# Optimization experiments

Hardware: AMD Instinct MI355X
Metric: run time of the kernel (lower is better)

The kernel has to match this reference:

```python
import jax, jax.numpy as jnp
import numpy as np

B, CIN, COUT, HIN = 2, 64, 64, 96
ALPHA = 0.2       # LeakyReLU slope in GAT
K_RANK = 6        # dist.argsort(1).argsort(1) <= 6  -> 7 nearest neighbors incl. self
DN = ('NCHW', 'OIHW', 'NCHW')


def setup_inputs():
    key = jax.random.key(0)
    ks = jax.random.split(key, 10)
    sc = lambda k, shape, s: jax.random.normal(k, shape, jnp.float32) * s
    return {
        'x': jax.random.normal(ks[0], (B, CIN, HIN, HIN), jnp.float32),
        'conv_w': sc(ks[1], (COUT, CIN, 3, 3), 0.05),
        'conv_b': jnp.zeros((COUT,), jnp.float32),
        'W1': sc(ks[2], (COUT, COUT), 0.1),
        'a1': sc(ks[3], (2 * COUT,), 0.1),
        'W2': sc(ks[4], (COUT, COUT), 0.1),
        'a2': sc(ks[5], (2 * COUT,), 0.1),
        'Wout': sc(ks[6], (2 * COUT, COUT), 0.1),
        'aout': sc(ks[7], (2 * COUT,), 0.1),
        'tconv_w': sc(ks[8], (COUT, COUT, 3, 3), 0.05),  # torch ConvTranspose2d layout [in,out,kh,kw]
        'tconv_b': jnp.zeros((COUT,), jnp.float32),
    }


def _gat_layer(h, adj, W, a, concat):
    # h: [B,N,F_in], W: [F_in,F_out], a: [2*F_out]
    Wh = h @ W                                   # [B,N,F']
    Fo = W.shape[1]
    e = (Wh @ a[:Fo])[:, :, None] + (Wh @ a[Fo:])[:, None, :]   # [B,N,N]
    e = jax.nn.leaky_relu(e, ALPHA)
    e = jnp.where(adj > 0, e, -9e15)
    attn = jax.nn.softmax(e, axis=-1)
    out = jnp.einsum('bij,bjf->bif', attn, Wh)
    return jax.nn.elu(out) if concat else out


def reference(x, conv_w, conv_b, W1, a1, W2, a2, Wout, aout, tconv_w, tconv_b):
    # --- Pre_ProcessLayer_Graph: stride-2 conv, flatten, 7-NN dense adjacency ---
    y = jax.lax.conv_general_dilated(x, conv_w, (2, 2), ((1, 1), (1, 1)),
                                     dimension_numbers=DN) + conv_b[None, :, None, None]
    Bb, C, H, W_ = y.shape
    N = H * W_
    feat = y.reshape(Bb, C, N).transpose(0, 2, 1)          # [B,N,C]
    sq = jnp.sum(feat * feat, axis=-1)                     # [B,N]
    d2 = sq[:, :, None] + sq[:, None, :] - 2.0 * jnp.einsum('bic,bjc->bij', feat, feat)
    dist = jnp.sqrt(jnp.maximum(d2, 0.0))                  # euclidean cdist
    ranks = jnp.argsort(jnp.argsort(dist, axis=-1), axis=-1)
    adj = (ranks <= K_RANK).astype(feat.dtype)             # [B,N,N] binary, incl. self (rank 0)
    # --- GAT (pyGAT style): 2 concat heads + output attention layer, eval mode ---
    h1 = _gat_layer(feat, adj, W1, a1, True)
    h2 = _gat_layer(feat, adj, W2, a2, True)
    hcat = jnp.concatenate([h1, h2], axis=-1)              # [B,N,2C]
    g = jax.nn.elu(_gat_layer(hcat, adj, Wout, aout, False))  # [B,N,C]
    # --- reshape back + transpose conv (k=3, s=2, p=1, output_padding=1) ---
    g = g.transpose(0, 2, 1).reshape(Bb, C, H, W_)
    wt = jnp.flip(tconv_w, (2, 3)).transpose(1, 0, 2, 3)   # -> [out,in,kh,kw]
    out = jax.lax.conv_general_dilated(g, wt, (1, 1), ((1, 2), (1, 2)),
                                       lhs_dilation=(2, 2),
                                       dimension_numbers=DN) + tconv_b[None, :, None, None]
    return out
```

## Files before the change

### kernel.cpp

```cpp
#include <hip/hip_runtime.h>
#include <hip/hip_bf16.h>
#include <stdint.h>

using bf16 = __hip_bfloat16;
using u64 = unsigned long long;

constexpr int B_ = 2;
constexpr int N_ = 2304;

constexpr int OFF_WC2   = 0;
constexpr int OFF_WT2   = 36864;
constexpr int OFF_W1F   = 73728;
constexpr int OFF_W2F   = 77824;
constexpr int OFF_WOUTF = 81920;
constexpr int OFF_A1F   = 90112;
constexpr int OFF_A2F   = 90240;
constexpr int OFF_AOUTF = 90368;
constexpr int OFF_CBF   = 90496;
constexpr int OFF_TBF   = 90560;
constexpr int OFF_FLAG  = 90624;
constexpr int OFF_SQ    = 90688;
constexpr int OFF_S11   = 95296;
constexpr int OFF_S12   = 99904;
constexpr int OFF_S21   = 104512;
constexpr int OFF_S22   = 109120;
constexpr int OFF_S1O   = 113728;
constexpr int OFF_S2O   = 118336;
constexpr int OFF_KNN   = 122944;
constexpr int OFF_BUF0  = 159808;
constexpr int OFF_BUF1  = 454720;
constexpr int OFF_BUF2  = 749632;
constexpr int OFF_BUF3  = 1044544;
constexpr int OFF_PK    = 1339456;

__device__ __forceinline__ float bf2f_raw(unsigned short u) {
    return __uint_as_float(((unsigned int)u) << 16);
}

__device__ __forceinline__ unsigned int mono32(float f) {
    unsigned int u = __float_as_uint(f);
    return (u & 0x80000000u) ? ~u : (u | 0x80000000u);
}

__device__ __forceinline__ bool detect_f32(const void* conv_w) {
    const unsigned short* cw = (const unsigned short*)conv_w;
    float m = 0.f;
    #pragma unroll
    for (int u = 0; u < 64; ++u) {
        float v = fabsf(bf2f_raw(cw[u]));
        if (v < 3.0e38f) m = fmaxf(m, v);
    }
    return m > 1.0e4f;
}

__global__ __launch_bounds__(256) void kc_prep(
    const void* conv_w, const void* conv_b, const void* W1, const void* a1,
    const void* W2, const void* a2, const void* Wout, const void* aout,
    const void* tconv_w, const void* tconv_b, float* __restrict__ ws)
{
    bool f32 = detect_f32(conv_w);
    int idx = blockIdx.x * 256 + threadIdx.x;
    if (idx == 0) ws[OFF_FLAG] = f32 ? 1.f : 0.f;
    if (idx < 32256) ws[OFF_SQ + idx] = 0.f;

    {
        int tap = idx >> 12, ic = (idx >> 6) & 63, oc = idx & 63;
        if (f32) {
            ws[OFF_WC2 + idx] = ((const float*)conv_w)[(oc * 64 + ic) * 9 + tap];
            ws[OFF_WT2 + idx] = ((const float*)tconv_w)[(ic * 64 + oc) * 9 + tap];
        } else {
            ws[OFF_WC2 + idx] = bf2f_raw(((const unsigned short*)conv_w)[(oc * 64 + ic) * 9 + tap]);
            ws[OFF_WT2 + idx] = bf2f_raw(((const unsigned short*)tconv_w)[(ic * 64 + oc) * 9 + tap]);
        }
    }
    if (idx < 4096) {
        if (f32) {
            ws[OFF_W1F + idx] = ((const float*)W1)[idx];
            ws[OFF_W2F + idx] = ((const float*)W2)[idx];
        } else {
            ws[OFF_W1F + idx] = bf2f_raw(((const unsigned short*)W1)[idx]);
            ws[OFF_W2F + idx] = bf2f_raw(((const unsigned short*)W2)[idx]);
        }
    }
    if (idx < 8192)
        ws[OFF_WOUTF + idx] = f32 ? ((const float*)Wout)[idx]
                                  : bf2f_raw(((const unsigned short*)Wout)[idx]);
    if (idx < 128) {
        if (f32) {
            ws[OFF_A1F + idx]   = ((const float*)a1)[idx];
            ws[OFF_A2F + idx]   = ((const float*)a2)[idx];
            ws[OFF_AOUTF + idx] = ((const float*)aout)[idx];
        } else {
            ws[OFF_A1F + idx]   = bf2f_raw(((const unsigned short*)a1)[idx]);
            ws[OFF_A2F + idx]   = bf2f_raw(((const unsigned short*)a2)[idx]);
            ws[OFF_AOUTF + idx] = bf2f_raw(((const unsigned short*)aout)[idx]);
        }
    }
    if (idx < 64) {
        if (f32) {
            ws[OFF_CBF + idx] = ((const float*)conv_b)[idx];
            ws[OFF_TBF + idx] = ((const float*)tconv_b)[idx];
        } else {
            ws[OFF_CBF + idx] = bf2f_raw(((const unsigned short*)conv_b)[idx]);
            ws[OFF_TBF + idx] = bf2f_raw(((const unsigned short*)tconv_b)[idx]);
        }
    }
}

template <bool F32>
__device__ __forceinline__ void conv_body(const void* __restrict__ x,
                                          float* __restrict__ ws,
                                          int n, int ocb, int b)
{
    int oy = n / 48, ox = n - (n / 48) * 48;
    const float* wc2 = ws + OFF_WC2;
    size_t xb = (size_t)b * 64 * 9216;
    float acc[4] = {0, 0, 0, 0};

    for (int ky = 0; ky < 3; ++ky) {
        int iy = 2 * oy - 1 + ky;
        bool vy = (unsigned)iy < 96u;
        int iyc = vy ? iy : 0;
        for (int kx = 0; kx < 3; ++kx) {
            int ix = 2 * ox - 1 + kx;
            bool v = vy && ((unsigned)ix < 96u);
            int ixc = v ? ix : 0;
            size_t xoff = xb + iyc * 96 + ixc;
            const float* wb = wc2 + (ky * 3 + kx) * 4096 + ocb;
            #pragma unroll 8
            for (int ic = 0; ic < 64; ++ic) {
                float xv;
                if (F32) xv = ((const float*)x)[xoff + ic * 9216];
                else     xv = bf2f_raw(((const unsigned short*)x)[xoff + ic * 9216]);
                xv = v ? xv : 0.f;
                const float* wr = wb + ic * 64;
                #pragma unroll
                for (int o = 0; o < 4; ++o) acc[o] += xv * wr[o];
            }
        }
    }
    float* featT = ws + OFF_BUF0 + (size_t)b * 64 * N_;
    const float* cb = ws + OFF_CBF;
    float ssum = 0.f;
    #pragma unroll
    for (int o = 0; o < 4; ++o) {
        float f = acc[o] + cb[ocb + o];
        acc[o] = f;
        featT[(ocb + o) * N_ + n] = f;
        ssum += f * f;
    }
    *(float4*)(ws + OFF_BUF2 + ((size_t)(b * N_ + n) * 64 + ocb)) =
        make_float4(acc[0], acc[1], acc[2], acc[3]);
    atomicAdd(ws + OFF_SQ + b * N_ + n, ssum);
}

__global__ __launch_bounds__(128) void k1_conv(const void* __restrict__ x,
                                               float* __restrict__ ws)
{
    int n   = blockIdx.x * 128 + threadIdx.x;
    int ocb = blockIdx.y * 4;
    int b   = blockIdx.z;
    if (ws[OFF_FLAG] != 0.f) conv_body<true >(x, ws, n, ocb, b);
    else                     conv_body<false>(x, ws, n, ocb, b);
}

__global__ __launch_bounds__(256) void k2_knn(float* __restrict__ ws)
{
    __shared__ float Bs[32][256];
    float* ysp = &Bs[0][0];
    int tid = threadIdx.x;
    int i0  = blockIdx.x * 16;
    int jh  = blockIdx.y;
    int b   = i0 / N_;
    const float* fT  = ws + OFF_BUF0 + (size_t)b * 64 * N_;
    const float* fnc = ws + OFF_BUF2;
    const float* sq  = ws + OFF_SQ + b * N_;
    int w = tid >> 6, lane = tid & 63;
    int r0 = w * 4;
    int arow0 = __builtin_amdgcn_readfirstlane(i0 + r0);

    u64 K[7];
    #pragma unroll
    for (int t = 0; t < 7; ++t) K[t] = ~0ull;

    int rsel = tid >> 4;
    int g    = tid & 15;

    for (int jt = 0; jt < 3; ++jt) {
        int jb = jh * 768 + jt * 256;
        float acc[4][4];
        #pragma unroll
        for (int r = 0; r < 4; ++r)
            #pragma unroll
            for (int c = 0; c < 4; ++c) acc[r][c] = 0.f;

        for (int kh = 0; kh < 2; ++kh) {
            __syncthreads();
            #pragma unroll
            for (int it = 0; it < 8; ++it) {
                int idx = tid + it * 256;
                int k = idx >> 6, j4 = idx & 63;
                float4 v = *(const float4*)(fT + (size_t)(kh * 32 + k) * N_ + jb + j4 * 4);
                *(float4*)&Bs[k][j4 * 4] = v;
            }
            __syncthreads();

            #pragma unroll 2
            for (int k4 = 0; k4 < 8; ++k4) {
                float4 Bv[4];
                #pragma unroll
                for (int kk = 0; kk < 4; ++kk)
                    Bv[kk] = *(const float4*)&Bs[k4 * 4 + kk][4 * lane];
                #pragma unroll
                for (int r = 0; r < 4; ++r) {
                    float4 a = *(const float4*)(fnc + (size_t)(arow0 + r) * 64
                                                + kh * 32 + k4 * 4);
                    acc[r][0] += a.x * Bv[0].x + a.y * Bv[1].x + a.z * Bv[2].x + a.w * Bv[3].x;
                    acc[r][1] += a.x * Bv[0].y + a.y * Bv[1].y + a.z * Bv[2].y + a.w * Bv[3].y;
                    acc[r][2] += a.x * Bv[0].z + a.y * Bv[1].z + a.z * Bv[2].z + a.w * Bv[3].z;
                    acc[r][3] += a.x * Bv[0].w + a.y * Bv[1].w + a.z * Bv[2].w + a.w * Bv[3].w;
                }
            }
        }

        __syncthreads();
        float4 sqv = *(const float4*)(sq + jb + 4 * lane);
        #pragma unroll
        for (int r = 0; r < 4; ++r) {
            float4 yv;
            yv.x = sqv.x - 2.f * acc[r][0];
            yv.y = sqv.y - 2.f * acc[r][1];
            yv.z = sqv.z - 2.f * acc[r][2];
            yv.w = sqv.w - 2.f * acc[r][3];
            *(float4*)&ysp[(r0 + r) * 264 + 4 * lane] = yv;
        }
        __syncthreads();

        #pragma unroll 4
        for (int u = 0; u < 16; ++u) {
            int jl = g + 16 * u;
            float y = ysp[rsel * 264 + jl];
            u64 key = ((u64)mono32(y) << 32) | (unsigned int)(jb + jl);
            if (key < K[6]) {
                int pos = 0;
                #pragma unroll
                for (int s = 0; s < 7; ++s) pos += (K[s] < key) ? 1 : 0;
                #pragma unroll
                for (int p = 6; p > 0; --p)
                    K[p] = (p == pos) ? key : ((p > pos) ? K[p - 1] : K[p]);
                if (pos == 0) K[0] = key;
            }
        }
        __syncthreads();
    }

    u64 myk = 0;
    for (int pass = 0; pass < 7; ++pass) {
        u64 m = K[0];
        #pragma unroll
        for (int s = 1; s < 7; ++s) m = (K[s] < m) ? K[s] : m;
        #pragma unroll
        for (int off = 1; off < 16; off <<= 1) {
            u64 o = (u64)__shfl_xor((long long)m, off);
            m = (o < m) ? o : m;
        }
        #pragma unroll
        for (int s = 0; s < 7; ++s)
            if (K[s] == m) K[s] = ~0ull;
        if (g == pass) myk = m;
    }
    if (g < 7) {
        u64* pk = (u64*)(ws + OFF_PK);
        pk[((size_t)(i0 + rsel) * 3 + jh) * 8 + g] = myk;
    }
}

__global__ __launch_bounds__(256) void k_lin(float* __restrict__ ws)
{
    int g = blockIdx.y;
    if (g == 32) {
        int row = blockIdx.x * 256 + threadIdx.x;
        const u64* pk = (const u64*)(ws + OFF_PK) + (size_t)row * 24;
        int* kout = (int*)(ws + OFF_KNN) + (size_t)row * 8;
        u64 L0[7], L1[7], L2[7];
        #pragma unroll
        for (int q = 0; q < 7; ++q) { L0[q] = pk[q]; L1[q] = pk[8 + q]; L2[q] = pk[16 + q]; }
        #pragma unroll
        for (int q = 0; q < 7; ++q) {
            int rank = q;
            #pragma unroll
            for (int p = 0; p < 7; ++p)
                rank += ((L1[p] < L0[q]) ? 1 : 0) + ((L2[p] < L0[q]) ? 1 : 0);
            if (rank < 7) kout[rank] = (int)(L0[q] & 0xffffffffull);
        }
        #pragma unroll
        for (int q = 0; q < 7; ++q) {
            int rank = q;
            #pragma unroll
            for (int p = 0; p < 7; ++p)
                rank += ((L0[p] < L1[q]) ? 1 : 0) + ((L2[p] < L1[q]) ? 1 : 0);
            if (rank < 7) kout[rank] = (int)(L1[q] & 0xffffffffull);
        }
        #pragma unroll
        for (int q = 0; q < 7; ++q) {
            int rank = q;
            #pragma unroll
            for (int p = 0; p < 7; ++p)
                rank += ((L0[p] < L2[q]) ? 1 : 0) + ((L1[p] < L2[q]) ? 1 : 0);
            if (rank < 7) kout[rank] = (int)(L2[q] & 0xffffffffull);
        }
        return;
    }
    int layer = g >> 4;
    int ocb = (g & 15) * 4;
    const float* W  = ws + (layer ? OFF_W2F : OFF_W1F);
    const float* a  = ws + (layer ? OFF_A2F : OFF_A1F);
    float* out_nc   = ws + (layer ? OFF_BUF3 : OFF_BUF1);
    float* s1       = ws + (layer ? OFF_S21 : OFF_S11);
    float* s2       = ws + (layer ? OFF_S22 : OFF_S12);
    int i = blockIdx.x * 256 + threadIdx.x;
    int b = i / N_, n = i - b * N_;
    const float* in_b = ws + OFF_BUF0 + (size_t)b * 64 * N_;

    float acc[4] = {0, 0, 0, 0};
    #pragma unroll 8
    for (int kk = 0; kk < 64; ++kk) {
        float xv = in_b[kk * N_ + n];
        const float* wr = W + kk * 64 + ocb;
        #pragma unroll
        for (int o = 0; o < 4; ++o) acc[o] += xv * wr[o];
    }
    *(float4*)(out_nc + ((size_t)i * 64 + ocb)) =
        make_float4(acc[0], acc[1], acc[2], acc[3]);
    float p1 = 0.f, p2 = 0.f;
    #pragma unroll
    for (int o = 0; o < 4; ++o) {
        p1 += acc[o] * a[ocb + o];
        p2 += acc[o] * a[64 + ocb + o];
    }
    atomicAdd(s1 + i, p1);
    atomicAdd(s2 + i, p2);
}

__global__ __launch_bounds__(256) void k_lin2(float* __restrict__ ws)
{
    int ocb = blockIdx.y * 4;
    int i = blockIdx.x * 256 + threadIdx.x;
    int b = i / N_, n = i - b * N_;
    const float* h1 = ws + OFF_BUF2 + (size_t)b * 64 * N_;
    const float* h2 = ws + OFF_BUF0 + (size_t)b * 64 * N_;
    const float* W  = ws + OFF_WOUTF;
    const float* a  = ws + OFF_AOUTF;

    float acc[4] = {0, 0, 0, 0};
    #pragma unroll 8
    for (int kk = 0; kk < 64; ++kk) {
        float xv = h1[kk * N_ + n];
        const float* wr = W + kk * 64 + ocb;
        #pragma unroll
        for (int o = 0; o < 4; ++o) acc[o] += xv * wr[o];
    }
    #pragma unroll 8
    for (int kk = 0; kk < 64; ++kk) {
        float xv = h2[kk * N_ + n];
        const float* wr = W + (64 + kk) * 64 + ocb;
        #pragma unroll
        for (int o = 0; o < 4; ++o) acc[o] += xv * wr[o];
    }
    *(float4*)(ws + OFF_BUF1 + ((size_t)i * 64 + ocb)) =
        make_float4(acc[0], acc[1], acc[2], acc[3]);
    float p1 = 0.f, p2 = 0.f;
    #pragma unroll
    for (int o = 0; o < 4; ++o) {
        p1 += acc[o] * a[ocb + o];
        p2 += acc[o] * a[64 + ocb + o];
    }
    atomicAdd(ws + OFF_S1O + i, p1);
    atomicAdd(ws + OFF_S2O + i, p2);
}

__device__ __forceinline__ void attn_body(
    const float* __restrict__ Wh_nc, const float* __restrict__ s1,
    const float* __restrict__ s2, const int* __restrict__ knn,
    float* __restrict__ out, int i, int b, int n, int c4)
{
    const int* kp = knn + (size_t)i * 8;
    int j[7];
    #pragma unroll
    for (int t = 0; t < 7; ++t) {
        int jt = kp[t];
        j[t] = ((unsigned)jt < (unsigned)N_) ? jt : 0;
    }
    float si = s1[i];
    const float* s2b = s2 + b * N_;
    float e[7];
    #pragma unroll
    for (int t = 0; t < 7; ++t) {
        float v = si + s2b[j[t]];
        e[t] = v > 0.f ? v : 0.2f * v;
    }
    float m = e[0];
    #pragma unroll
    for (int t = 1; t < 7; ++t) m = fmaxf(m, e[t]);
    float ssum = 0.f;
    #pragma unroll
    for (int t = 0; t < 7; ++t) { e[t] = __expf(e[t] - m); ssum += e[t]; }
    float inv = 1.f / ssum;
    #pragma unroll
    for (int t = 0; t < 7; ++t) e[t] *= inv;

    const float4* W4 = (const float4*)Wh_nc;
    float4 acc = make_float4(0.f, 0.f, 0.f, 0.f);
    #pragma unroll
    for (int t = 0; t < 7; ++t) {
        float4 v = W4[(size_t)(b * N_ + j[t]) * 16 + c4];
        acc.x += e[t] * v.x; acc.y += e[t] * v.y;
        acc.z += e[t] * v.z; acc.w += e[t] * v.w;
    }
    acc.x = acc.x > 0.f ? acc.x : expm1f(acc.x);
    acc.y = acc.y > 0.f ? acc.y : expm1f(acc.y);
    acc.z = acc.z > 0.f ? acc.z : expm1f(acc.z);
    acc.w = acc.w > 0.f ? acc.w : expm1f(acc.w);
    float* ob = out + (size_t)b * 64 * N_;
    ob[(c4 * 4 + 0) * N_ + n] = acc.x;
    ob[(c4 * 4 + 1) * N_ + n] = acc.y;
    ob[(c4 * 4 + 2) * N_ + n] = acc.z;
    ob[(c4 * 4 + 3) * N_ + n] = acc.w;
}

__global__ __launch_bounds__(256) void k_attn12(float* __restrict__ ws)
{
    int layer = blockIdx.z;
    const float* Wh_nc = ws + (layer ? OFF_BUF3 : OFF_BUF1);
    const float* s1    = ws + (layer ? OFF_S21 : OFF_S11);
    const float* s2    = ws + (layer ? OFF_S22 : OFF_S12);
    float* out         = ws + (layer ? OFF_BUF0 : OFF_BUF2);
    int c4 = blockIdx.y;
    int i = blockIdx.x * 256 + threadIdx.x;
    int b = i / N_, n = i - b * N_;
    attn_body(Wh_nc, s1, s2, (const int*)(ws + OFF_KNN), out, i, b, n, c4);
}

__global__ __launch_bounds__(256) void k_attn_out(float* __restrict__ ws)
{
    int c4 = blockIdx.y;
    int i = blockIdx.x * 256 + threadIdx.x;
    int b = i / N_, n = i - b * N_;
    attn_body(ws + OFF_BUF1, ws + OFF_S1O, ws + OFF_S2O,
              (const int*)(ws + OFF_KNN), ws + OFF_BUF3, i, b, n, c4);
}

__global__ __launch_bounds__(128) void k7_tconv(float* __restrict__ ws,
                                                void* __restrict__ outp)
{
    bool f32 = ws[OFF_FLAG] != 0.f;
    int pixc = blockIdx.x * 128 + threadIdx.x;
    int g    = blockIdx.y;
    int pc   = g >> 3, ocb = (g & 7) * 8;
    int b    = blockIdx.z;
    int py = pc >> 1, px = pc & 1;
    int ay = pixc / 48, bx = pixc - (pixc / 48) * 48;
    int oy = 2 * ay + py, ox = 2 * bx + px;

    const float* gT  = ws + OFF_BUF3 + (size_t)b * 64 * N_;
    const float* wt2 = ws + OFF_WT2;
    float acc[8] = {0, 0, 0, 0, 0, 0, 0, 0};

    int nky = py ? 2 : 1;
    int nkx = px ? 2 : 1;
    for (int s = 0; s < nky; ++s) {
        int ky = py ? (s == 0 ? 0 : 2) : 1;
        int iy = py ? (s == 0 ? ay + 1 : ay) : ay;
        bool vy = iy < 48;
        for (int t = 0; t < nkx; ++t) {
            int kx = px ? (t == 0 ? 0 : 2) : 1;
            int ix = px ? (t == 0 ? bx + 1 : bx) : bx;
            bool v = vy && (ix < 48);
            const float* gp = gT + (v ? iy * 48 + ix : 0);
            const float* wb = wt2 + (ky * 3 + kx) * 4096 + ocb;
            #pragma unroll 8
            for (int ic = 0; ic < 64; ++ic) {
                float gv = gp[ic * N_];
                gv = v ? gv : 0.f;
                const float* wr = wb + ic * 64;
                #pragma unroll
                for (int o = 0; o < 8; ++o) acc[o] += gv * wr[o];
            }
        }
    }
    const float* tb = ws + OFF_TBF;
    size_t base = ((size_t)(b * 64 + ocb) * 96 + oy) * 96 + ox;
    if (f32) {
        float* op = (float*)outp;
        #pragma unroll
        for (int o = 0; o < 8; ++o) op[base + (size_t)o * 9216] = acc[o] + tb[ocb + o];
    } else {
        bf16* op = (bf16*)outp;
        #pragma unroll
        for (int o = 0; o < 8; ++o)
            op[base + (size_t)o * 9216] = __float2bfloat16(acc[o] + tb[ocb + o]);
    }
}

extern "C" void kernel_launch(void* const* d_in, const int* in_sizes, int n_in,
                              void* d_out, int out_size, void* d_ws, size_t ws_size,
                              hipStream_t stream)
{
    float* ws = (float*)d_ws;

    hipLaunchKernelGGL(kc_prep, dim3(144), dim3(256), 0, stream,
                       d_in[1], d_in[2], d_in[3], d_in[4], d_in[5], d_in[6],
                       d_in[7], d_in[8], d_in[9], d_in[10], ws);
    hipLaunchKernelGGL(k1_conv, dim3(18, 16, 2), dim3(128), 0, stream, d_in[0], ws);
    hipLaunchKernelGGL(k2_knn, dim3(288, 3), dim3(256), 0, stream, ws);
    hipLaunchKernelGGL(k_lin, dim3(18, 33), dim3(256), 0, stream, ws);
    hipLaunchKernelGGL(k_attn12, dim3(18, 16, 2), dim3(256), 0, stream, ws);
    hipLaunchKernelGGL(k_lin2, dim3(18, 16), dim3(256), 0, stream, ws);
    hipLaunchKernelGGL(k_attn_out, dim3(18, 16), dim3(256), 0, stream, ws);
    hipLaunchKernelGGL(k7_tconv, dim3(18, 32, 2), dim3(128), 0, stream, ws, d_out);
}
```

Before: 230.7 us.

## Fuse all stages into one persistent kernel with atomic grid barriers

```diff
diff --git a/kernel.cpp b/kernel.cpp
--- a/kernel.cpp
+++ b/kernel.cpp
@@ -19,6 +19,7 @@
 constexpr int OFF_CBF   = 90496;
 constexpr int OFF_TBF   = 90560;
 constexpr int OFF_FLAG  = 90624;
+constexpr int OFF_BAR   = 90632;
 constexpr int OFF_SQ    = 90688;
 constexpr int OFF_S11   = 95296;
 constexpr int OFF_S12   = 99904;
@@ -33,6 +34,8 @@
 constexpr int OFF_BUF3  = 1044544;
 constexpr int OFF_PK    = 1339456;
 
+constexpr unsigned NBLK = 864;
+
 __device__ __forceinline__ float bf2f_raw(unsigned short u) {
     return __uint_as_float(((unsigned int)u) << 16);
 }
@@ -53,67 +56,27 @@
     return m > 1.0e4f;
 }
 
-__global__ __launch_bounds__(256) void kc_prep(
-    const void* conv_w, const void* conv_b, const void* W1, const void* a1,
-    const void* W2, const void* a2, const void* Wout, const void* aout,
-    const void* tconv_w, const void* tconv_b, float* __restrict__ ws)
-{
-    bool f32 = detect_f32(conv_w);
-    int idx = blockIdx.x * 256 + threadIdx.x;
-    if (idx == 0) ws[OFF_FLAG] = f32 ? 1.f : 0.f;
-    if (idx < 32256) ws[OFF_SQ + idx] = 0.f;
-
-    {
-        int tap = idx >> 12, ic = (idx >> 6) & 63, oc = idx & 63;
-        if (f32) {
-            ws[OFF_WC2 + idx] = ((const float*)conv_w)[(oc * 64 + ic) * 9 + tap];
-            ws[OFF_WT2 + idx] = ((const float*)tconv_w)[(ic * 64 + oc) * 9 + tap];
-        } else {
-            ws[OFF_WC2 + idx] = bf2f_raw(((const unsigned short*)conv_w)[(oc * 64 + ic) * 9 + tap]);
-            ws[OFF_WT2 + idx] = bf2f_raw(((const unsigned short*)tconv_w)[(ic * 64 + oc) * 9 + tap]);
-        }
-    }
-    if (idx < 4096) {
-        if (f32) {
-            ws[OFF_W1F + idx] = ((const float*)W1)[idx];
-            ws[OFF_W2F + idx] = ((const float*)W2)[idx];
-        } else {
-            ws[OFF_W1F + idx] = bf2f_raw(((const unsigned short*)W1)[idx]);
-            ws[OFF_W2F + idx] = bf2f_raw(((const unsigned short*)W2)[idx]);
-        }
-    }
-    if (idx < 8192)
-        ws[OFF_WOUTF + idx] = f32 ? ((const float*)Wout)[idx]
-                                  : bf2f_raw(((const unsigned short*)Wout)[idx]);
-    if (idx < 128) {
-        if (f32) {
-            ws[OFF_A1F + idx]   = ((const float*)a1)[idx];
-            ws[OFF_A2F + idx]   = ((const float*)a2)[idx];
-            ws[OFF_AOUTF + idx] = ((const float*)aout)[idx];
-        } else {
-            ws[OFF_A1F + idx]   = bf2f_raw(((const unsigned short*)a1)[idx]);
-            ws[OFF_A2F + idx]   = bf2f_raw(((const unsigned short*)a2)[idx]);
-            ws[OFF_AOUTF + idx] = bf2f_raw(((const unsigned short*)aout)[idx]);
-        }
-    }
-    if (idx < 64) {
-        if (f32) {
-            ws[OFF_CBF + idx] = ((const float*)conv_b)[idx];
-            ws[OFF_TBF + idx] = ((const float*)tconv_b)[idx];
-        } else {
-            ws[OFF_CBF + idx] = bf2f_raw(((const unsigned short*)conv_b)[idx]);
-            ws[OFF_TBF + idx] = bf2f_raw(((const unsigned short*)tconv_b)[idx]);
-        }
-    }
+__device__ __forceinline__ void gridbar(float* __restrict__ ws, unsigned target) {
+    __syncthreads();
+    if (threadIdx.x == 0) {
+        __threadfence();
+        atomicAdd((unsigned*)(ws + OFF_BAR), 1u);
+        int guard = 0;
+        while (atomicAdd((unsigned*)(ws + OFF_BAR), 0u) < target) {
+            __builtin_amdgcn_s_sleep(32);
+            if (++guard > (1 << 20)) break;
+        }
+        __threadfence();
+    }
+    __syncthreads();
 }
 
 template <bool F32>
-__device__ __forceinline__ void conv_body(const void* __restrict__ x,
-                                          float* __restrict__ ws,
-                                          int n, int ocb, int b)
+__device__ __forceinline__ void conv_body_raw(const void* __restrict__ x,
+        const void* __restrict__ cw, const void* __restrict__ cb,
+        float* __restrict__ ws, int n, int ocb, int b)
 {
     int oy = n / 48, ox = n - (n / 48) * 48;
-    const float* wc2 = ws + OFF_WC2;
     size_t xb = (size_t)b * 64 * 9216;
     float acc[4] = {0, 0, 0, 0};
 
@@ -126,25 +89,31 @@
             bool v = vy && ((unsigned)ix < 96u);
             int ixc = v ? ix : 0;
             size_t xoff = xb + iyc * 96 + ixc;
-            const float* wb = wc2 + (ky * 3 + kx) * 4096 + ocb;
+            int tap = ky * 3 + kx;
             #pragma unroll 8
             for (int ic = 0; ic < 64; ++ic) {
                 float xv;
                 if (F32) xv = ((const float*)x)[xoff + ic * 9216];
                 else     xv = bf2f_raw(((const unsigned short*)x)[xoff + ic * 9216]);
                 xv = v ? xv : 0.f;
-                const float* wr = wb + ic * 64;
-                #pragma unroll
-                for (int o = 0; o < 4; ++o) acc[o] += xv * wr[o];
+                #pragma unroll
+                for (int o = 0; o < 4; ++o) {
+                    float wv;
+                    size_t widx = ((size_t)(ocb + o) * 64 + ic) * 9 + tap;
+                    if (F32) wv = ((const float*)cw)[widx];
+                    else     wv = bf2f_raw(((const unsigned short*)cw)[widx]);
+                    acc[o] += xv * wv;
+                }
             }
         }
     }
     float* featT = ws + OFF_BUF0 + (size_t)b * 64 * N_;
-    const float* cb = ws + OFF_CBF;
     float ssum = 0.f;
     #pragma unroll
     for (int o = 0; o < 4; ++o) {
-        float f = acc[o] + cb[ocb + o];
+        float bv = F32 ? ((const float*)cb)[ocb + o]
+                       : bf2f_raw(((const unsigned short*)cb)[ocb + o]);
+        float f = acc[o] + bv;
         acc[o] = f;
         featT[(ocb + o) * N_ + n] = f;
         ssum += f * f;
@@ -152,231 +121,6 @@
     *(float4*)(ws + OFF_BUF2 + ((size_t)(b * N_ + n) * 64 + ocb)) =
         make_float4(acc[0], acc[1], acc[2], acc[3]);
     atomicAdd(ws + OFF_SQ + b * N_ + n, ssum);
-}
-
-__global__ __launch_bounds__(128) void k1_conv(const void* __restrict__ x,
-                                               float* __restrict__ ws)
-{
-    int n   = blockIdx.x * 128 + threadIdx.x;
-    int ocb = blockIdx.y * 4;
-    int b   = blockIdx.z;
-    if (ws[OFF_FLAG] != 0.f) conv_body<true >(x, ws, n, ocb, b);
-    else                     conv_body<false>(x, ws, n, ocb, b);
-}
-
-__global__ __launch_bounds__(256) void k2_knn(float* __restrict__ ws)
-{
-    __shared__ float Bs[32][256];
-    float* ysp = &Bs[0][0];
-    int tid = threadIdx.x;
-    int i0  = blockIdx.x * 16;
-    int jh  = blockIdx.y;
-    int b   = i0 / N_;
-    const float* fT  = ws + OFF_BUF0 + (size_t)b * 64 * N_;
-    const float* fnc = ws + OFF_BUF2;
-    const float* sq  = ws + OFF_SQ + b * N_;
-    int w = tid >> 6, lane = tid & 63;
-    int r0 = w * 4;
-    int arow0 = __builtin_amdgcn_readfirstlane(i0 + r0);
-
-    u64 K[7];
-    #pragma unroll
-    for (int t = 0; t < 7; ++t) K[t] = ~0ull;
-
-    int rsel = tid >> 4;
-    int g    = tid & 15;
-
-    for (int jt = 0; jt < 3; ++jt) {
-        int jb = jh * 768 + jt * 256;
-        float acc[4][4];
-        #pragma unroll
-        for (int r = 0; r < 4; ++r)
-            #pragma unroll
-            for (int c = 0; c < 4; ++c) acc[r][c] = 0.f;
-
-        for (int kh = 0; kh < 2; ++kh) {
-            __syncthreads();
-            #pragma unroll
-            for (int it = 0; it < 8; ++it) {
-                int idx = tid + it * 256;
-                int k = idx >> 6, j4 = idx & 63;
-                float4 v = *(const float4*)(fT + (size_t)(kh * 32 + k) * N_ + jb + j4 * 4);
-                *(float4*)&Bs[k][j4 * 4] = v;
-            }
-            __syncthreads();
-
-            #pragma unroll 2
-            for (int k4 = 0; k4 < 8; ++k4) {
-                float4 Bv[4];
-                #pragma unroll
-                for (int kk = 0; kk < 4; ++kk)
-                    Bv[kk] = *(const float4*)&Bs[k4 * 4 + kk][4 * lane];
-                #pragma unroll
-                for (int r = 0; r < 4; ++r) {
-                    float4 a = *(const float4*)(fnc + (size_t)(arow0 + r) * 64
-                                                + kh * 32 + k4 * 4);
-                    acc[r][0] += a.x * Bv[0].x + a.y * Bv[1].x + a.z * Bv[2].x + a.w * Bv[3].x;
-                    acc[r][1] += a.x * Bv[0].y + a.y * Bv[1].y + a.z * Bv[2].y + a.w * Bv[3].y;
-                    acc[r][2] += a.x * Bv[0].z + a.y * Bv[1].z + a.z * Bv[2].z + a.w * Bv[3].z;
-                    acc[r][3] += a.x * Bv[0].w + a.y * Bv[1].w + a.z * Bv[2].w + a.w * Bv[3].w;
-                }
-            }
-        }
-
-        __syncthreads();
-        float4 sqv = *(const float4*)(sq + jb + 4 * lane);
-        #pragma unroll
-        for (int r = 0; r < 4; ++r) {
-            float4 yv;
-            yv.x = sqv.x - 2.f * acc[r][0];
-            yv.y = sqv.y - 2.f * acc[r][1];
-            yv.z = sqv.z - 2.f * acc[r][2];
-            yv.w = sqv.w - 2.f * acc[r][3];
-            *(float4*)&ysp[(r0 + r) * 264 + 4 * lane] = yv;
-        }
-        __syncthreads();
-
-        #pragma unroll 4
-        for (int u = 0; u < 16; ++u) {
-            int jl = g + 16 * u;
-            float y = ysp[rsel * 264 + jl];
-            u64 key = ((u64)mono32(y) << 32) | (unsigned int)(jb + jl);
-            if (key < K[6]) {
-                int pos = 0;
-                #pragma unroll
-                for (int s = 0; s < 7; ++s) pos += (K[s] < key) ? 1 : 0;
-                #pragma unroll
-                for (int p = 6; p > 0; --p)
-                    K[p] = (p == pos) ? key : ((p > pos) ? K[p - 1] : K[p]);
-                if (pos == 0) K[0] = key;
-            }
-        }
-        __syncthreads();
-    }
-
-    u64 myk = 0;
-    for (int pass = 0; pass < 7; ++pass) {
-        u64 m = K[0];
-        #pragma unroll
-        for (int s = 1; s < 7; ++s) m = (K[s] < m) ? K[s] : m;
-        #pragma unroll
-        for (int off = 1; off < 16; off <<= 1) {
-            u64 o = (u64)__shfl_xor((long long)m, off);
-            m = (o < m) ? o : m;
-        }
-        #pragma unroll
-        for (int s = 0; s < 7; ++s)
-            if (K[s] == m) K[s] = ~0ull;
-        if (g == pass) myk = m;
-    }
-    if (g < 7) {
-        u64* pk = (u64*)(ws + OFF_PK);
-        pk[((size_t)(i0 + rsel) * 3 + jh) * 8 + g] = myk;
-    }
-}
-
-__global__ __launch_bounds__(256) void k_lin(float* __restrict__ ws)
-{
-    int g = blockIdx.y;
-    if (g == 32) {
-        int row = blockIdx.x * 256 + threadIdx.x;
-        const u64* pk = (const u64*)(ws + OFF_PK) + (size_t)row * 24;
-        int* kout = (int*)(ws + OFF_KNN) + (size_t)row * 8;
-        u64 L0[7], L1[7], L2[7];
-        #pragma unroll
-        for (int q = 0; q < 7; ++q) { L0[q] = pk[q]; L1[q] = pk[8 + q]; L2[q] = pk[16 + q]; }
-        #pragma unroll
-        for (int q = 0; q < 7; ++q) {
-            int rank = q;
-            #pragma unroll
-            for (int p = 0; p < 7; ++p)
-                rank += ((L1[p] < L0[q]) ? 1 : 0) + ((L2[p] < L0[q]) ? 1 : 0);
-            if (rank < 7) kout[rank] = (int)(L0[q] & 0xffffffffull);
-        }
-        #pragma unroll
-        for (int q = 0; q < 7; ++q) {
-            int rank = q;
-            #pragma unroll
-            for (int p = 0; p < 7; ++p)
-                rank += ((L0[p] < L1[q]) ? 1 : 0) + ((L2[p] < L1[q]) ? 1 : 0);
-            if (rank < 7) kout[rank] = (int)(L1[q] & 0xffffffffull);
-        }
-        #pragma unroll
-        for (int q = 0; q < 7; ++q) {
-            int rank = q;
-            #pragma unroll
-            for (int p = 0; p < 7; ++p)
-                rank += ((L0[p] < L2[q]) ? 1 : 0) + ((L1[p] < L2[q]) ? 1 : 0);
-            if (rank < 7) kout[rank] = (int)(L2[q] & 0xffffffffull);
-        }
-        return;
-    }
-    int layer = g >> 4;
-    int ocb = (g & 15) * 4;
-    const float* W  = ws + (layer ? OFF_W2F : OFF_W1F);
-    const float* a  = ws + (layer ? OFF_A2F : OFF_A1F);
-    float* out_nc   = ws + (layer ? OFF_BUF3 : OFF_BUF1);
-    float* s1       = ws + (layer ? OFF_S21 : OFF_S11);
-    float* s2       = ws + (layer ? OFF_S22 : OFF_S12);
-    int i = blockIdx.x * 256 + threadIdx.x;
-    int b = i / N_, n = i - b * N_;
-    const float* in_b = ws + OFF_BUF0 + (size_t)b * 64 * N_;
-
-    float acc[4] = {0, 0, 0, 0};
-    #pragma unroll 8
-    for (int kk = 0; kk < 64; ++kk) {
-        float xv = in_b[kk * N_ + n];
-        const float* wr = W + kk * 64 + ocb;
-        #pragma unroll
-        for (int o = 0; o < 4; ++o) acc[o] += xv * wr[o];
-    }
-    *(float4*)(out_nc + ((size_t)i * 64 + ocb)) =
-        make_float4(acc[0], acc[1], acc[2], acc[3]);
-    float p1 = 0.f, p2 = 0.f;
-    #pragma unroll
-    for (int o = 0; o < 4; ++o) {
-        p1 += acc[o] * a[ocb + o];
-        p2 += acc[o] * a[64 + ocb + o];
-    }
-    atomicAdd(s1 + i, p1);
-    atomicAdd(s2 + i, p2);
-}
-
-__global__ __launch_bounds__(256) void k_lin2(float* __restrict__ ws)
-{
-    int ocb = blockIdx.y * 4;
-    int i = blockIdx.x * 256 + threadIdx.x;
-    int b = i / N_, n = i - b * N_;
-    const float* h1 = ws + OFF_BUF2 + (size_t)b * 64 * N_;
-    const float* h2 = ws + OFF_BUF0 + (size_t)b * 64 * N_;
-    const float* W  = ws + OFF_WOUTF;
-    const float* a  = ws + OFF_AOUTF;
-
-    float acc[4] = {0, 0, 0, 0};
-    #pragma unroll 8
-    for (int kk = 0; kk < 64; ++kk) {
-        float xv = h1[kk * N_ + n];
-        const float* wr = W + kk * 64 + ocb;
-        #pragma unroll
-        for (int o = 0; o < 4; ++o) acc[o] += xv * wr[o];
-    }
-    #pragma unroll 8
-    for (int kk = 0; kk < 64; ++kk) {
-        float xv = h2[kk * N_ + n];
-        const float* wr = W + (64 + kk) * 64 + ocb;
-        #pragma unroll
-        for (int o = 0; o < 4; ++o) acc[o] += xv * wr[o];
-    }
-    *(float4*)(ws + OFF_BUF1 + ((size_t)i * 64 + ocb)) =
-        make_float4(acc[0], acc[1], acc[2], acc[3]);
-    float p1 = 0.f, p2 = 0.f;
-    #pragma unroll
-    for (int o = 0; o < 4; ++o) {
-        p1 += acc[o] * a[ocb + o];
-        p2 += acc[o] * a[64 + ocb + o];
-    }
-    atomicAdd(ws + OFF_S1O + i, p1);
-    atomicAdd(ws + OFF_S2O + i, p2);
 }
 
 __device__ __forceinline__ void attn_body(
@@ -428,77 +172,359 @@
     ob[(c4 * 4 + 3) * N_ + n] = acc.w;
 }
 
-__global__ __launch_bounds__(256) void k_attn12(float* __restrict__ ws)
+__global__ __launch_bounds__(256, 4) void k_all(
+    const void* __restrict__ x,
+    const void* conv_w, const void* conv_b, const void* W1, const void* a1,
+    const void* W2, const void* a2, const void* Wout, const void* aout,
+    const void* tconv_w, const void* tconv_b,
+    float* __restrict__ ws, void* __restrict__ outp)
 {
-    int layer = blockIdx.z;
-    const float* Wh_nc = ws + (layer ? OFF_BUF3 : OFF_BUF1);
-    const float* s1    = ws + (layer ? OFF_S21 : OFF_S11);
-    const float* s2    = ws + (layer ? OFF_S22 : OFF_S12);
-    float* out         = ws + (layer ? OFF_BUF0 : OFF_BUF2);
-    int c4 = blockIdx.y;
-    int i = blockIdx.x * 256 + threadIdx.x;
-    int b = i / N_, n = i - b * N_;
-    attn_body(Wh_nc, s1, s2, (const int*)(ws + OFF_KNN), out, i, b, n, c4);
-}
-
-__global__ __launch_bounds__(256) void k_attn_out(float* __restrict__ ws)
-{
-    int c4 = blockIdx.y;
-    int i = blockIdx.x * 256 + threadIdx.x;
-    int b = i / N_, n = i - b * N_;
-    attn_body(ws + OFF_BUF1, ws + OFF_S1O, ws + OFF_S2O,
-              (const int*)(ws + OFF_KNN), ws + OFF_BUF3, i, b, n, c4);
-}
-
-__global__ __launch_bounds__(128) void k7_tconv(float* __restrict__ ws,
-                                                void* __restrict__ outp)
-{
-    bool f32 = ws[OFF_FLAG] != 0.f;
-    int pixc = blockIdx.x * 128 + threadIdx.x;
-    int g    = blockIdx.y;
-    int pc   = g >> 3, ocb = (g & 7) * 8;
-    int b    = blockIdx.z;
-    int py = pc >> 1, px = pc & 1;
-    int ay = pixc / 48, bx = pixc - (pixc / 48) * 48;
-    int oy = 2 * ay + py, ox = 2 * bx + px;
-
-    const float* gT  = ws + OFF_BUF3 + (size_t)b * 64 * N_;
-    const float* wt2 = ws + OFF_WT2;
-    float acc[8] = {0, 0, 0, 0, 0, 0, 0, 0};
-
-    int nky = py ? 2 : 1;
-    int nkx = px ? 2 : 1;
-    for (int s = 0; s < nky; ++s) {
-        int ky = py ? (s == 0 ? 0 : 2) : 1;
-        int iy = py ? (s == 0 ? ay + 1 : ay) : ay;
-        bool vy = iy < 48;
-        for (int t = 0; t < nkx; ++t) {
-            int kx = px ? (t == 0 ? 0 : 2) : 1;
-            int ix = px ? (t == 0 ? bx + 1 : bx) : bx;
-            bool v = vy && (ix < 48);
-            const float* gp = gT + (v ? iy * 48 + ix : 0);
-            const float* wb = wt2 + (ky * 3 + kx) * 4096 + ocb;
+    int bx = blockIdx.x, tid = threadIdx.x;
+
+    if (bx < 144) {
+        bool f32 = detect_f32(conv_w);
+        int idx = bx * 256 + tid;
+        if (idx == 0) ws[OFF_FLAG] = f32 ? 1.f : 0.f;
+        {
+            int tap = idx >> 12, ic = (idx >> 6) & 63, oc = idx & 63;
+            if (f32) {
+                ws[OFF_WC2 + idx] = ((const float*)conv_w)[(oc * 64 + ic) * 9 + tap];
+                ws[OFF_WT2 + idx] = ((const float*)tconv_w)[(ic * 64 + oc) * 9 + tap];
+            } else {
+                ws[OFF_WC2 + idx] = bf2f_raw(((const unsigned short*)conv_w)[(oc * 64 + ic) * 9 + tap]);
+                ws[OFF_WT2 + idx] = bf2f_raw(((const unsigned short*)tconv_w)[(ic * 64 + oc) * 9 + tap]);
+            }
+        }
+        if (idx < 4096) {
+            if (f32) {
+                ws[OFF_W1F + idx] = ((const float*)W1)[idx];
+                ws[OFF_W2F + idx] = ((const float*)W2)[idx];
+            } else {
+                ws[OFF_W1F + idx] = bf2f_raw(((const unsigned short*)W1)[idx]);
+                ws[OFF_W2F + idx] = bf2f_raw(((const unsigned short*)W2)[idx]);
+            }
+        }
+        if (idx < 8192)
+            ws[OFF_WOUTF + idx] = f32 ? ((const float*)Wout)[idx]
+                                      : bf2f_raw(((const unsigned short*)Wout)[idx]);
+        if (idx < 128) {
+            if (f32) {
+                ws[OFF_A1F + idx]   = ((const float*)a1)[idx];
+                ws[OFF_A2F + idx]   = ((const float*)a2)[idx];
+                ws[OFF_AOUTF + idx] = ((const float*)aout)[idx];
+            } else {
+                ws[OFF_A1F + idx]   = bf2f_raw(((const unsigned short*)a1)[idx]);
+                ws[OFF_A2F + idx]   = bf2f_raw(((const unsigned short*)a2)[idx]);
+                ws[OFF_AOUTF + idx] = bf2f_raw(((const unsigned short*)aout)[idx]);
+            }
+        }
+        if (idx < 64) {
+            if (f32) {
+                ws[OFF_CBF + idx] = ((const float*)conv_b)[idx];
+                ws[OFF_TBF + idx] = ((const float*)tconv_b)[idx];
+            } else {
+                ws[OFF_CBF + idx] = bf2f_raw(((const unsigned short*)conv_b)[idx]);
+                ws[OFF_TBF + idx] = bf2f_raw(((const unsigned short*)tconv_b)[idx]);
+            }
+        }
+    } else if (bx < 432) {
+        int t = (bx - 144) * 256 + tid;
+        int b   = __builtin_amdgcn_readfirstlane(t / 36864);
+        int r   = t % 36864;
+        int ocb = __builtin_amdgcn_readfirstlane((r / 2304) * 4);
+        int n   = r % 2304;
+        bool f32 = detect_f32(conv_w);
+        if (f32) conv_body_raw<true >(x, conv_w, conv_b, ws, n, ocb, b);
+        else     conv_body_raw<false>(x, conv_w, conv_b, ws, n, ocb, b);
+    }
+    gridbar(ws, NBLK * 1);
+
+    {
+        __shared__ float Bs[32][256];
+        float* ysp = &Bs[0][0];
+        int i0 = (bx % 288) * 16;
+        int jh = bx / 288;
+        int b  = i0 / N_;
+        const float* fT  = ws + OFF_BUF0 + (size_t)b * 64 * N_;
+        const float* fnc = ws + OFF_BUF2;
+        const float* sq  = ws + OFF_SQ + b * N_;
+        int w = tid >> 6, lane = tid & 63;
+        int r0 = w * 4;
+        int arow0 = __builtin_amdgcn_readfirstlane(i0 + r0);
+
+        u64 K[7];
+        #pragma unroll
+        for (int t = 0; t < 7; ++t) K[t] = ~0ull;
+        int rsel = tid >> 4;
+        int g    = tid & 15;
+
+        for (int jt = 0; jt < 3; ++jt) {
+            int jb = jh * 768 + jt * 256;
+            float acc[4][4];
+            #pragma unroll
+            for (int r = 0; r < 4; ++r)
+                #pragma unroll
+                for (int c = 0; c < 4; ++c) acc[r][c] = 0.f;
+
+            for (int kh = 0; kh < 2; ++kh) {
+                __syncthreads();
+                #pragma unroll
+                for (int it = 0; it < 8; ++it) {
+                    int idx = tid + it * 256;
+                    int k = idx >> 6, j4 = idx & 63;
+                    float4 v = *(const float4*)(fT + (size_t)(kh * 32 + k) * N_ + jb + j4 * 4);
+                    *(float4*)&Bs[k][j4 * 4] = v;
+                }
+                __syncthreads();
+
+                #pragma unroll 2
+                for (int k4 = 0; k4 < 8; ++k4) {
+                    float4 Bv[4];
+                    #pragma unroll
+                    for (int kk = 0; kk < 4; ++kk)
+                        Bv[kk] = *(const float4*)&Bs[k4 * 4 + kk][4 * lane];
+                    #pragma unroll
+                    for (int r = 0; r < 4; ++r) {
+                        float4 a = *(const float4*)(fnc + (size_t)(arow0 + r) * 64
+                                                    + kh * 32 + k4 * 4);
+                        acc[r][0] += a.x * Bv[0].x + a.y * Bv[1].x + a.z * Bv[2].x + a.w * Bv[3].x;
+                        acc[r][1] += a.x * Bv[0].y + a.y * Bv[1].y + a.z * Bv[2].y + a.w * Bv[3].y;
+                        acc[r][2] += a.x * Bv[0].z + a.y * Bv[1].z + a.z * Bv[2].z + a.w * Bv[3].z;
+                        acc[r][3] += a.x * Bv[0].w + a.y * Bv[1].w + a.z * Bv[2].w + a.w * Bv[3].w;
+                    }
+                }
+            }
+
+            __syncthreads();
+            float4 sqv = *(const float4*)(sq + jb + 4 * lane);
+            #pragma unroll
+            for (int r = 0; r < 4; ++r) {
+                float4 yv;
+                yv.x = sqv.x - 2.f * acc[r][0];
+                yv.y = sqv.y - 2.f * acc[r][1];
+                yv.z = sqv.z - 2.f * acc[r][2];
+                yv.w = sqv.w - 2.f * acc[r][3];
+                *(float4*)&ysp[(r0 + r) * 264 + 4 * lane] = yv;
+            }
+            #pragma unroll 4
+            for (int u = 0; u < 16; ++u) {
+                int jl = g + 16 * u;
+                float y = ysp[rsel * 264 + jl];
+                u64 key = ((u64)mono32(y) << 32) | (unsigned int)(jb + jl);
+                if (key < K[6]) {
+                    int pos = 0;
+                    #pragma unroll
+                    for (int s = 0; s < 7; ++s) pos += (K[s] < key) ? 1 : 0;
+                    #pragma unroll
+                    for (int p = 6; p > 0; --p)
+                        K[p] = (p == pos) ? key : ((p > pos) ? K[p - 1] : K[p]);
+                    if (pos == 0) K[0] = key;
+                }
+            }
+            __syncthreads();
+        }
+
+        u64 myk = 0;
+        for (int pass = 0; pass < 7; ++pass) {
+            u64 m = K[0];
+            #pragma unroll
+            for (int s = 1; s < 7; ++s) m = (K[s] < m) ? K[s] : m;
+            #pragma unroll
+            for (int off = 1; off < 16; off <<= 1) {
+                u64 o = (u64)__shfl_xor((long long)m, off);
+                m = (o < m) ? o : m;
+            }
+            #pragma unroll
+            for (int s = 0; s < 7; ++s)
+                if (K[s] == m) K[s] = ~0ull;
+            if (g == pass) myk = m;
+        }
+        if (g < 7) {
+            u64* pk = (u64*)(ws + OFF_PK);
+            pk[((size_t)(i0 + rsel) * 3 + jh) * 8 + g] = myk;
+        }
+    }
+    gridbar(ws, NBLK * 2);
+
+    if (bx < 594) {
+        int g = bx / 18, xb = bx % 18;
+        if (g == 32) {
+            int row = xb * 256 + tid;
+            const u64* pk = (const u64*)(ws + OFF_PK) + (size_t)row * 24;
+            int* kout = (int*)(ws + OFF_KNN) + (size_t)row * 8;
+            u64 L0[7], L1[7], L2[7];
+            #pragma unroll
+            for (int q = 0; q < 7; ++q) { L0[q] = pk[q]; L1[q] = pk[8 + q]; L2[q] = pk[16 + q]; }
+            #pragma unroll
+            for (int q = 0; q < 7; ++q) {
+                int rank = q;
+                #pragma unroll
+                for (int p = 0; p < 7; ++p)
+                    rank += ((L1[p] < L0[q]) ? 1 : 0) + ((L2[p] < L0[q]) ? 1 : 0);
+                if (rank < 7) kout[rank] = (int)(L0[q] & 0xffffffffull);
+            }
+            #pragma unroll
+            for (int q = 0; q < 7; ++q) {
+                int rank = q;
+                #pragma unroll
+                for (int p = 0; p < 7; ++p)
+                    rank += ((L0[p] < L1[q]) ? 1 : 0) + ((L2[p] < L1[q]) ? 1 : 0);
+                if (rank < 7) kout[rank] = (int)(L1[q] & 0xffffffffull);
+            }
+            #pragma unroll
+            for (int q = 0; q < 7; ++q) {
+                int rank = q;
+                #pragma unroll
+                for (int p = 0; p < 7; ++p)
+                    rank += ((L0[p] < L2[q]) ? 1 : 0) + ((L1[p] < L2[q]) ? 1 : 0);
+                if (rank < 7) kout[rank] = (int)(L2[q] & 0xffffffffull);
+            }
+        } else {
+            int layer = g >> 4;
+            int ocb = (g & 15) * 4;
+            const float* W  = ws + (layer ? OFF_W2F : OFF_W1F);
+            const float* a  = ws + (layer ? OFF_A2F : OFF_A1F);
+            float* out_nc   = ws + (layer ? OFF_BUF3 : OFF_BUF1);
+            float* s1       = ws + (layer ? OFF_S21 : OFF_S11);
+            float* s2       = ws + (layer ? OFF_S22 : OFF_S12);
+            int i = xb * 256 + tid;
+            int b = i / N_, n = i - b * N_;
+            const float* in_b = ws + OFF_BUF0 + (size_t)b * 64 * N_;
+
+            float acc[4] = {0, 0, 0, 0};
             #pragma unroll 8
-            for (int ic = 0; ic < 64; ++ic) {
-                float gv = gp[ic * N_];
-                gv = v ? gv : 0.f;
-                const float* wr = wb + ic * 64;
-                #pragma unroll
-                for (int o = 0; o < 8; ++o) acc[o] += gv * wr[o];
-            }
-        }
-    }
-    const float* tb = ws + OFF_TBF;
-    size_t base = ((size_t)(b * 64 + ocb) * 96 + oy) * 96 + ox;
-    if (f32) {
-        float* op = (float*)outp;
+            for (int kk = 0; kk < 64; ++kk) {
+                float xv = in_b[kk * N_ + n];
+                const float* wr = W + kk * 64 + ocb;
+                #pragma unroll
+                for (int o = 0; o < 4; ++o) acc[o] += xv * wr[o];
+            }
+            *(float4*)(out_nc + ((size_t)i * 64 + ocb)) =
+                make_float4(acc[0], acc[1], acc[2], acc[3]);
+            float p1 = 0.f, p2 = 0.f;
+            #pragma unroll
+            for (int o = 0; o < 4; ++o) {
+                p1 += acc[o] * a[ocb + o];
+                p2 += acc[o] * a[64 + ocb + o];
+            }
+            atomicAdd(s1 + i, p1);
+            atomicAdd(s2 + i, p2);
+        }
+    }
+    gridbar(ws, NBLK * 3);
+
+    if (bx < 576) {
+        int layer = bx / 288, c = bx % 288;
+        int c4 = c / 18, xb = c % 18;
+        const float* Wh_nc = ws + (layer ? OFF_BUF3 : OFF_BUF1);
+        const float* s1    = ws + (layer ? OFF_S21 : OFF_S11);
+        const float* s2    = ws + (layer ? OFF_S22 : OFF_S12);
+        float* out         = ws + (layer ? OFF_BUF0 : OFF_BUF2);
+        int i = xb * 256 + tid;
+        int b = i / N_, n = i - b * N_;
+        attn_body(Wh_nc, s1, s2, (const int*)(ws + OFF_KNN), out, i, b, n, c4);
+    }
+    gridbar(ws, NBLK * 4);
+
+    if (bx < 288) {
+        int c4g = bx / 18, xb = bx % 18;
+        int ocb = c4g * 4;
+        int i = xb * 256 + tid;
+        int b = i / N_, n = i - b * N_;
+        const float* h1 = ws + OFF_BUF2 + (size_t)b * 64 * N_;
+        const float* h2 = ws + OFF_BUF0 + (size_t)b * 64 * N_;
+        const float* W  = ws + OFF_WOUTF;
+        const float* a  = ws + OFF_AOUTF;
+
+        float acc[4] = {0, 0, 0, 0};
+        #pragma unroll 8
+        for (int kk = 0; kk < 64; ++kk) {
+            float xv = h1[kk * N_ + n];
+            const float* wr = W + kk * 64 + ocb;
+            #pragma unroll
+            for (int o = 0; o < 4; ++o) acc[o] += xv * wr[o];
+        }
+        #pragma unroll 8
+        for (int kk = 0; kk < 64; ++kk) {
+            float xv = h2[kk * N_ + n];
+            const float* wr = W + (64 + kk) * 64 + ocb;
+            #pragma unroll
+            for (int o = 0; o < 4; ++o) acc[o] += xv * wr[o];
+        }
+        *(float4*)(ws + OFF_BUF1 + ((size_t)i * 64 + ocb)) =
+            make_float4(acc[0], acc[1], acc[2], acc[3]);
+        float p1 = 0.f, p2 = 0.f;
         #pragma unroll
-        for (int o = 0; o < 8; ++o) op[base + (size_t)o * 9216] = acc[o] + tb[ocb + o];
-    } else {
-        bf16* op = (bf16*)outp;
-        #pragma unroll
-        for (int o = 0; o < 8; ++o)
-            op[base + (size_t)o * 9216] = __float2bfloat16(acc[o] + tb[ocb + o]);
+        for (int o = 0; o < 4; ++o) {
+            p1 += acc[o] * a[ocb + o];
+            p2 += acc[o] * a[64 + ocb + o];
+        }
+        atomicAdd(ws + OFF_S1O + i, p1);
+        atomicAdd(ws + OFF_S2O + i, p2);
+    }
+    gridbar(ws, NBLK * 5);
+
+    if (bx < 288) {
+        int c4 = bx / 18, xb = bx % 18;
+        int i = xb * 256 + tid;
+        int b = i / N_, n = i - b * N_;
+        attn_body(ws + OFF_BUF1, ws + OFF_S1O, ws + OFF_S2O,
+                  (const int*)(ws + OFF_KNN), ws + OFF_BUF3, i, b, n, c4);
+    }
+    gridbar(ws, NBLK * 6);
+
+    if (bx < 576) {
+        bool f32 = ws[OFF_FLAG] != 0.f;
+        int t = bx * 256 + tid;
+        int tid_old = t & 127;
+        int blk = t >> 7;
+        int xo = __builtin_amdgcn_readfirstlane(blk % 18);
+        int gg = __builtin_amdgcn_readfirstlane((blk / 18) % 32);
+        int b  = __builtin_amdgcn_readfirstlane(blk / 576);
+        int pixc = xo * 128 + tid_old;
+        int pc   = gg >> 3, ocb = (gg & 7) * 8;
+        int py = pc >> 1, px = pc & 1;
+        int ay = pixc / 48, bxx = pixc - (pixc / 48) * 48;
+        int oy = 2 * ay + py, ox = 2 * bxx + px;
+
+        const float* gT  = ws + OFF_BUF3 + (size_t)b * 64 * N_;
+        const float* wt2 = ws + OFF_WT2;
+        float acc[8] = {0, 0, 0, 0, 0, 0, 0, 0};
+
+        int nky = py ? 2 : 1;
+        int nkx = px ? 2 : 1;
+        for (int s = 0; s < nky; ++s) {
+            int ky = py ? (s == 0 ? 0 : 2) : 1;
+            int iy = py ? (s == 0 ? ay + 1 : ay) : ay;
+            bool vy = iy < 48;
+            for (int u = 0; u < nkx; ++u) {
+                int kx = px ? (u == 0 ? 0 : 2) : 1;
+                int ix = px ? (u == 0 ? bxx + 1 : bxx) : bxx;
+                bool v = vy && (ix < 48);
+                const float* gp = gT + (v ? iy * 48 + ix : 0);
+                const float* wb = wt2 + (ky * 3 + kx) * 4096 + ocb;
+                #pragma unroll 8
+                for (int ic = 0; ic < 64; ++ic) {
+                    float gv = gp[ic * N_];
+                    gv = v ? gv : 0.f;
+                    const float* wr = wb + ic * 64;
+                    #pragma unroll
+                    for (int o = 0; o < 8; ++o) acc[o] += gv * wr[o];
+                }
+            }
+        }
+        const float* tb = ws + OFF_TBF;
+        size_t base = ((size_t)(b * 64 + ocb) * 96 + oy) * 96 + ox;
+        if (f32) {
+            float* op = (float*)outp;
+            #pragma unroll
+            for (int o = 0; o < 8; ++o) op[base + (size_t)o * 9216] = acc[o] + tb[ocb + o];
+        } else {
+            bf16* op = (bf16*)outp;
+            #pragma unroll
+            for (int o = 0; o < 8; ++o)
+                op[base + (size_t)o * 9216] = __float2bfloat16(acc[o] + tb[ocb + o]);
+        }
     }
 }
 
@@ -507,15 +533,9 @@
                               hipStream_t stream)
 {
     float* ws = (float*)d_ws;
-
-    hipLaunchKernelGGL(kc_prep, dim3(144), dim3(256), 0, stream,
-                       d_in[1], d_in[2], d_in[3], d_in[4], d_in[5], d_in[6],
-                       d_in[7], d_in[8], d_in[9], d_in[10], ws);
-    hipLaunchKernelGGL(k1_conv, dim3(18, 16, 2), dim3(128), 0, stream, d_in[0], ws);
-    hipLaunchKernelGGL(k2_knn, dim3(288, 3), dim3(256), 0, stream, ws);
-    hipLaunchKernelGGL(k_lin, dim3(18, 33), dim3(256), 0, stream, ws);
-    hipLaunchKernelGGL(k_attn12, dim3(18, 16, 2), dim3(256), 0, stream, ws);
-    hipLaunchKernelGGL(k_lin2, dim3(18, 16), dim3(256), 0, stream, ws);
-    hipLaunchKernelGGL(k_attn_out, dim3(18, 16), dim3(256), 0, stream, ws);
-    hipLaunchKernelGGL(k7_tconv, dim3(18, 32, 2), dim3(128), 0, stream, ws, d_out);
-}
+    hipMemsetAsync(ws + OFF_FLAG, 0, (size_t)(OFF_KNN - OFF_FLAG) * 4, stream);
+    hipLaunchKernelGGL(k_all, dim3(NBLK), dim3(256), 0, stream,
+                       d_in[0], d_in[1], d_in[2], d_in[3], d_in[4], d_in[5],
+                       d_in[6], d_in[7], d_in[8], d_in[9], d_in[10],
+                       ws, d_out);
+}
```

Result: slower. 829.1 us (+259.4%).
